# Kernel optimization log

Measured on AMD Instinct MI355X. Metric: run time of the kernel, lower is better.

## Reference

```python
import jax, jax.numpy as jnp
import numpy as np
from jax.scipy.special import betaln

B, T = 4096, 8192

def setup_inputs() -> dict:
    key = jax.random.key(0)
    k_obs, k_a1, k_b1, k_a2, k_b2 = jax.random.split(key, 5)
    obs_seq = (jax.random.uniform(k_obs, (B, T)) < 0.5).astype(jnp.float32)
    # priors strictly positive, away from 0 to keep betaln finite
    alpha1 = jax.random.uniform(k_a1, (B,)) * 2.0 + 0.5
    beta1 = jax.random.uniform(k_b1, (B,)) * 2.0 + 0.5
    alpha2 = jax.random.uniform(k_a2, (B,)) * 2.0 + 0.5
    beta2 = jax.random.uniform(k_b2, (B,)) * 2.0 + 0.5
    mixweight = jnp.float32(0.4)
    return {"obs_seq": obs_seq, "alpha1": alpha1, "beta1": beta1,
            "alpha2": alpha2, "beta2": beta2, "mixweight": mixweight}

def reference(obs_seq, alpha1, beta1, alpha2, beta2, mixweight):
    # cumulative successes/failures, shifted right by one (posterior BEFORE obs t)
    cs = jnp.cumsum(obs_seq, axis=1)          # [B,T]
    cf = jnp.cumsum(1.0 - obs_seq, axis=1)    # [B,T]
    s_prev = jnp.pad(cs[:, :-1], ((0, 0), (1, 0)))  # cat([0, cs[:-1]])
    f_prev = jnp.pad(cf[:, :-1], ((0, 0), (1, 0)))
    a1 = alpha1[:, None] + s_prev
    b1 = beta1[:, None] + f_prev
    a2 = alpha2[:, None] + s_prev
    b2 = beta2[:, None] + f_prev
    clog1 = betaln(a1, b1) - betaln(alpha1, beta1)[:, None]
    clog2 = betaln(a2, b2) - betaln(alpha2, beta2)[:, None]
    bigconst = -clog1
    c1 = mixweight * jnp.exp(clog1 + bigconst)
    c2 = (1.0 - mixweight) * jnp.exp(clog2 + bigconst)
    post_mixweight = c1 / (c1 + c2)
    # stack the post_dict entries into one [5,B,T] array
    return jnp.stack([a1, b1, a2, b2, post_mixweight])
```

## Files before the change

### kernel.cpp

```cpp
#include <hip/hip_runtime.h>


#define BLOCK 256
#define VEC 4
#define NW (BLOCK / 64)

typedef float v4f __attribute__((ext_vector_type(4)));

__global__ __launch_bounds__(BLOCK) void bbm_kernel(
    const float* __restrict__ obs,
    const float* __restrict__ alpha1, const float* __restrict__ beta1,
    const float* __restrict__ alpha2, const float* __restrict__ beta2,
    const float* __restrict__ mixw,
    float* __restrict__ out,
    int T, size_t bt)
{
    const int bid   = blockIdx.x;
    const int row   = bid / 5;
    const int plane = bid - row * 5;
    const int tid   = threadIdx.x;
    const int lane  = tid & 63;
    const int wid   = tid >> 6;

    __shared__ int   sPart[2][NW];
    __shared__ float dPart[2][NW];

    const float* __restrict__ orow = obs + (size_t)row * T;
    float* __restrict__ prow = out + (size_t)plane * bt + (size_t)row * T;

    const unsigned long long lt_mask = ((unsigned long long)1 << lane) - 1ull;

    const int EPB   = BLOCK * VEC;
    const int iters = T / EPB;

    v4f cur = *(const v4f*)(orow + tid * VEC);

    if (plane < 4) {
        const float A1 = alpha1[row], B1 = beta1[row];
        const float A2 = alpha2[row], B2 = beta2[row];
        const float c0 = (plane == 0) ? A1 : (plane == 1) ? B1
                       : (plane == 2) ? A2 : B2;
        const bool use_s = (plane & 1) == 0;

        int carry_s = 0;
        for (int it = 0; it < iters; ++it) {
            const int t0 = it * EPB + tid * VEC;
            const int pb = it & 1;

            v4f nxt;
            if (it + 1 < iters) nxt = *(const v4f*)(orow + (it + 1) * EPB + tid * VEC);

            int bit[VEC], sloc[VEC];
            int ts = 0;
            #pragma unroll
            for (int j = 0; j < VEC; ++j) { bit[j] = cur[j] > 0.5f; sloc[j] = ts; ts += bit[j]; }

            unsigned long long m0 = __ballot(bit[0]);
            unsigned long long m1 = __ballot(bit[1]);
            unsigned long long m2 = __ballot(bit[2]);
            unsigned long long m3 = __ballot(bit[3]);
            const int wave_excl = __builtin_popcountll(m0 & lt_mask)
                                + __builtin_popcountll(m1 & lt_mask)
                                + __builtin_popcountll(m2 & lt_mask)
                                + __builtin_popcountll(m3 & lt_mask);
            const int wave_tot  = __builtin_popcountll(m0) + __builtin_popcountll(m1)
                                + __builtin_popcountll(m2) + __builtin_popcountll(m3);
            if (lane == 0) sPart[pb][wid] = wave_tot;
            __syncthreads();
            int prior = 0, total = 0;
            #pragma unroll
            for (int wI = 0; wI < NW; ++wI) {
                int p = sPart[pb][wI];
                total += p;
                if (wI < wid) prior += p;
            }
            const int tbase_s = carry_s + prior + wave_excl;

            v4f o;
            #pragma unroll
            for (int j = 0; j < VEC; ++j) {
                const float ft = (float)(t0 + j);
                const float fs = (float)(tbase_s + sloc[j]);
                o[j] = use_s ? (c0 + fs) : (c0 + (ft - fs));
            }
            *(v4f*)(prow + t0) = o;

            carry_s += total;
            cur = nxt;
        }
    } else {
        const float A1 = alpha1[row], B1 = beta1[row];
        const float A2 = alpha2[row], B2 = beta2[row];
        const float w  = mixw[0];
        const float AB1 = A1 + B1, AB2 = A2 + B2;
        const float w2 = 1.0f - w;

        int   carry_s = 0;
        float carry_d = 0.0f;

        for (int it = 0; it < iters; ++it) {
            const int t0 = it * EPB + tid * VEC;
            const int pb = it & 1;

            v4f nxt;
            if (it + 1 < iters) nxt = *(const v4f*)(orow + (it + 1) * EPB + tid * VEC);

            int bit[VEC], sloc[VEC];
            int ts = 0;
            #pragma unroll
            for (int j = 0; j < VEC; ++j) { bit[j] = cur[j] > 0.5f; sloc[j] = ts; ts += bit[j]; }

            unsigned long long m0 = __ballot(bit[0]);
            unsigned long long m1 = __ballot(bit[1]);
            unsigned long long m2 = __ballot(bit[2]);
            unsigned long long m3 = __ballot(bit[3]);
            const int wave_excl = __builtin_popcountll(m0 & lt_mask)
                                + __builtin_popcountll(m1 & lt_mask)
                                + __builtin_popcountll(m2 & lt_mask)
                                + __builtin_popcountll(m3 & lt_mask);
            const int wave_tot  = __builtin_popcountll(m0) + __builtin_popcountll(m1)
                                + __builtin_popcountll(m2) + __builtin_popcountll(m3);
            if (lane == 0) sPart[pb][wid] = wave_tot;
            __syncthreads();
            int prior = 0, total = 0;
            #pragma unroll
            for (int wI = 0; wI < NW; ++wI) {
                int p = sPart[pb][wI];
                total += p;
                if (wI < wid) prior += p;
            }
            const int tbase_s = carry_s + prior + wave_excl;

            float dloc[VEC];
            float td = 0.0f;
            #pragma unroll
            for (int j = 0; j < VEC; ++j) {
                const float ft = (float)(t0 + j);
                const float fs = (float)(tbase_s + sloc[j]);
                const float fp = ft - fs;
                const float sel1 = bit[j] ? (A1 + fs) : (B1 + fp);
                const float sel2 = bit[j] ? (A2 + fs) : (B2 + fp);
                const float delta = __logf(sel2 * (AB1 + ft)) - __logf(sel1 * (AB2 + ft));
                dloc[j] = td;
                td += delta;
            }

            float incl_d = td;
            #pragma unroll
            for (int off = 1; off < 64; off <<= 1) {
                float n = __shfl_up(incl_d, off, 64);
                if (lane >= off) incl_d += n;
            }
            if (lane == 63) dPart[pb][wid] = incl_d;
            __syncthreads();
            float priord = 0.0f, totald = 0.0f;
            #pragma unroll
            for (int wI = 0; wI < NW; ++wI) {
                float p = dPart[pb][wI];
                totald += p;
                if (wI < wid) priord += p;
            }
            const float tbase_d = carry_d + priord + (incl_d - td);

            v4f o;
            #pragma unroll
            for (int j = 0; j < VEC; ++j) {
                const float d = tbase_d + dloc[j];
                o[j] = __fdividef(w, w + w2 * __expf(d));
            }
            *(v4f*)(prow + t0) = o;

            carry_s += total;
            carry_d += totald;
            cur = nxt;
        }
    }
}

extern "C" void kernel_launch(void* const* d_in, const int* in_sizes, int n_in,
                              void* d_out, int out_size, void* d_ws, size_t ws_size,
                              hipStream_t stream) {
    const float* obs    = (const float*)d_in[0];
    const float* alpha1 = (const float*)d_in[1];
    const float* beta1  = (const float*)d_in[2];
    const float* alpha2 = (const float*)d_in[3];
    const float* beta2  = (const float*)d_in[4];
    const float* mixw   = (const float*)d_in[5];

    const int Bn = in_sizes[1];
    const int Tn = in_sizes[0] / Bn;
    const size_t bt = (size_t)Bn * (size_t)Tn;

    bbm_kernel<<<Bn * 5, BLOCK, 0, stream>>>(obs, alpha1, beta1, alpha2, beta2,
                                             mixw, (float*)d_out, Tn, bt);
}
```

Baseline: 795.4 us.

## Fuse five output planes into one block per row with staggered plane stores

Instead of launching five blocks per row that each redo the scan and write one plane, one block per row now computes all five outputs. This removes four redundant reads of obs and repeated scans. A templated fully unrolled variant for T equal to 8 segments delays each plane's store by a different number of segments, so the concurrent stores are spread across planes and addresses. The cost is fewer blocks in the grid (B instead of 5B), more live registers for the delayed buffers, and a heavier sequential chain per block.

```diff
diff --git a/kernel.cpp b/kernel.cpp
--- a/kernel.cpp
+++ b/kernel.cpp
@@ -7,7 +7,8 @@
 
 typedef float v4f __attribute__((ext_vector_type(4)));
 
-__global__ __launch_bounds__(BLOCK) void bbm_kernel(
+template <int SEGS>
+__global__ __launch_bounds__(BLOCK) void bbm_lag(
     const float* __restrict__ obs,
     const float* __restrict__ alpha1, const float* __restrict__ beta1,
     const float* __restrict__ alpha2, const float* __restrict__ beta2,
@@ -15,40 +16,44 @@
     float* __restrict__ out,
     int T, size_t bt)
 {
-    const int bid   = blockIdx.x;
-    const int row   = bid / 5;
-    const int plane = bid - row * 5;
-    const int tid   = threadIdx.x;
-    const int lane  = tid & 63;
-    const int wid   = tid >> 6;
+    const int row  = blockIdx.x;
+    const int tid  = threadIdx.x;
+    const int lane = tid & 63;
+    const int wid  = tid >> 6;
 
     __shared__ int   sPart[2][NW];
     __shared__ float dPart[2][NW];
 
+    const float A1 = alpha1[row], B1 = beta1[row];
+    const float A2 = alpha2[row], B2 = beta2[row];
+    const float w  = mixw[0];
+    const float AB1 = A1 + B1, AB2 = A2 + B2;
+    const float w2 = 1.0f - w;
+
     const float* __restrict__ orow = obs + (size_t)row * T;
-    float* __restrict__ prow = out + (size_t)plane * bt + (size_t)row * T;
+    float* __restrict__ obase = out + (size_t)row * T;
 
     const unsigned long long lt_mask = ((unsigned long long)1 << lane) - 1ull;
 
-    const int EPB   = BLOCK * VEC;
-    const int iters = T / EPB;
+    int   carry_s = 0;
+    float carry_d = 0.0f;
+
+    const int EPB = BLOCK * VEC;
+
+    v4f fb1[1], fa2[2], fb2[3], fpm[4];
 
     v4f cur = *(const v4f*)(orow + tid * VEC);
 
-    if (plane < 4) {
-        const float A1 = alpha1[row], B1 = beta1[row];
-        const float A2 = alpha2[row], B2 = beta2[row];
-        const float c0 = (plane == 0) ? A1 : (plane == 1) ? B1
-                       : (plane == 2) ? A2 : B2;
-        const bool use_s = (plane & 1) == 0;
-
-        int carry_s = 0;
-        for (int it = 0; it < iters; ++it) {
-            const int t0 = it * EPB + tid * VEC;
-            const int pb = it & 1;
+    #pragma unroll
+    for (int s = 0; s < SEGS + 4; ++s) {
+        v4f va1, vb1n, va2n, vb2n, vpmn;
+
+        if (s < SEGS) {
+            const int t0 = s * EPB + tid * VEC;
+            const int pb = s & 1;
 
             v4f nxt;
-            if (it + 1 < iters) nxt = *(const v4f*)(orow + (it + 1) * EPB + tid * VEC);
+            if (s + 1 < SEGS) nxt = *(const v4f*)(orow + (s + 1) * EPB + tid * VEC);
 
             int bit[VEC], sloc[VEC];
             int ts = 0;
@@ -76,61 +81,6 @@
             }
             const int tbase_s = carry_s + prior + wave_excl;
 
-            v4f o;
-            #pragma unroll
-            for (int j = 0; j < VEC; ++j) {
-                const float ft = (float)(t0 + j);
-                const float fs = (float)(tbase_s + sloc[j]);
-                o[j] = use_s ? (c0 + fs) : (c0 + (ft - fs));
-            }
-            *(v4f*)(prow + t0) = o;
-
-            carry_s += total;
-            cur = nxt;
-        }
-    } else {
-        const float A1 = alpha1[row], B1 = beta1[row];
-        const float A2 = alpha2[row], B2 = beta2[row];
-        const float w  = mixw[0];
-        const float AB1 = A1 + B1, AB2 = A2 + B2;
-        const float w2 = 1.0f - w;
-
-        int   carry_s = 0;
-        float carry_d = 0.0f;
-
-        for (int it = 0; it < iters; ++it) {
-            const int t0 = it * EPB + tid * VEC;
-            const int pb = it & 1;
-
-            v4f nxt;
-            if (it + 1 < iters) nxt = *(const v4f*)(orow + (it + 1) * EPB + tid * VEC);
-
-            int bit[VEC], sloc[VEC];
-            int ts = 0;
-            #pragma unroll
-            for (int j = 0; j < VEC; ++j) { bit[j] = cur[j] > 0.5f; sloc[j] = ts; ts += bit[j]; }
-
-            unsigned long long m0 = __ballot(bit[0]);
-            unsigned long long m1 = __ballot(bit[1]);
-            unsigned long long m2 = __ballot(bit[2]);
-            unsigned long long m3 = __ballot(bit[3]);
-            const int wave_excl = __builtin_popcountll(m0 & lt_mask)
-                                + __builtin_popcountll(m1 & lt_mask)
-                                + __builtin_popcountll(m2 & lt_mask)
-                                + __builtin_popcountll(m3 & lt_mask);
-            const int wave_tot  = __builtin_popcountll(m0) + __builtin_popcountll(m1)
-                                + __builtin_popcountll(m2) + __builtin_popcountll(m3);
-            if (lane == 0) sPart[pb][wid] = wave_tot;
-            __syncthreads();
-            int prior = 0, total = 0;
-            #pragma unroll
-            for (int wI = 0; wI < NW; ++wI) {
-                int p = sPart[pb][wI];
-                total += p;
-                if (wI < wid) prior += p;
-            }
-            const int tbase_s = carry_s + prior + wave_excl;
-
             float dloc[VEC];
             float td = 0.0f;
             #pragma unroll
@@ -162,18 +112,165 @@
             }
             const float tbase_d = carry_d + priord + (incl_d - td);
 
-            v4f o;
             #pragma unroll
             for (int j = 0; j < VEC; ++j) {
-                const float d = tbase_d + dloc[j];
-                o[j] = __fdividef(w, w + w2 * __expf(d));
-            }
-            *(v4f*)(prow + t0) = o;
+                const float ft = (float)(t0 + j);
+                const float fs = (float)(tbase_s + sloc[j]);
+                const float fp = ft - fs;
+                const float d  = tbase_d + dloc[j];
+                va1[j]  = A1 + fs;
+                vb1n[j] = B1 + fp;
+                va2n[j] = A2 + fs;
+                vb2n[j] = B2 + fp;
+                vpmn[j] = __fdividef(w, w + w2 * __expf(d));
+            }
+            *(v4f*)(obase + t0) = va1;
 
             carry_s += total;
             carry_d += totald;
             cur = nxt;
         }
+
+        if (s - 1 >= 0 && s - 1 < SEGS)
+            *(v4f*)(obase + bt     + (size_t)(s - 1) * EPB + tid * VEC) = fb1[0];
+        if (s - 2 >= 0 && s - 2 < SEGS)
+            *(v4f*)(obase + 2 * bt + (size_t)(s - 2) * EPB + tid * VEC) = fa2[s & 1];
+        if (s - 3 >= 0 && s - 3 < SEGS)
+            *(v4f*)(obase + 3 * bt + (size_t)(s - 3) * EPB + tid * VEC) = fb2[s % 3];
+        if (s - 4 >= 0 && s - 4 < SEGS)
+            *(v4f*)(obase + 4 * bt + (size_t)(s - 4) * EPB + tid * VEC) = fpm[s & 3];
+
+        if (s < SEGS) {
+            fb1[0]     = vb1n;
+            fa2[s & 1] = va2n;
+            fb2[s % 3] = vb2n;
+            fpm[s & 3] = vpmn;
+        }
+    }
+}
+
+__global__ __launch_bounds__(BLOCK) void bbm_kernel(
+    const float* __restrict__ obs,
+    const float* __restrict__ alpha1, const float* __restrict__ beta1,
+    const float* __restrict__ alpha2, const float* __restrict__ beta2,
+    const float* __restrict__ mixw,
+    float* __restrict__ out,
+    int T, size_t bt)
+{
+    const int row  = blockIdx.x;
+    const int tid  = threadIdx.x;
+    const int lane = tid & 63;
+    const int wid  = tid >> 6;
+
+    __shared__ int   sPart[2][NW];
+    __shared__ float dPart[2][NW];
+
+    const float A1 = alpha1[row], B1 = beta1[row];
+    const float A2 = alpha2[row], B2 = beta2[row];
+    const float w  = mixw[0];
+    const float AB1 = A1 + B1, AB2 = A2 + B2;
+    const float w2 = 1.0f - w;
+
+    const float* __restrict__ orow = obs + (size_t)row * T;
+    float* __restrict__ obase = out + (size_t)row * T;
+
+    const unsigned long long lt_mask = ((unsigned long long)1 << lane) - 1ull;
+
+    int   carry_s = 0;
+    float carry_d = 0.0f;
+
+    const int EPB  = BLOCK * VEC;
+    const int segs = T / EPB;
+
+    v4f cur = *(const v4f*)(orow + tid * VEC);
+
+    for (int s = 0; s < segs; ++s) {
+        const int t0 = s * EPB + tid * VEC;
+        const int pb = s & 1;
+
+        v4f nxt;
+        if (s + 1 < segs) nxt = *(const v4f*)(orow + (s + 1) * EPB + tid * VEC);
+
+        int bit[VEC], sloc[VEC];
+        int ts = 0;
+        #pragma unroll
+        for (int j = 0; j < VEC; ++j) { bit[j] = cur[j] > 0.5f; sloc[j] = ts; ts += bit[j]; }
+
+        unsigned long long m0 = __ballot(bit[0]);
+        unsigned long long m1 = __ballot(bit[1]);
+        unsigned long long m2 = __ballot(bit[2]);
+        unsigned long long m3 = __ballot(bit[3]);
+        const int wave_excl = __builtin_popcountll(m0 & lt_mask)
+                            + __builtin_popcountll(m1 & lt_mask)
+                            + __builtin_popcountll(m2 & lt_mask)
+                            + __builtin_popcountll(m3 & lt_mask);
+        const int wave_tot  = __builtin_popcountll(m0) + __builtin_popcountll(m1)
+                            + __builtin_popcountll(m2) + __builtin_popcountll(m3);
+        if (lane == 0) sPart[pb][wid] = wave_tot;
+        __syncthreads();
+        int prior = 0, total = 0;
+        #pragma unroll
+        for (int wI = 0; wI < NW; ++wI) {
+            int p = sPart[pb][wI];
+            total += p;
+            if (wI < wid) prior += p;
+        }
+        const int tbase_s = carry_s + prior + wave_excl;
+
+        float dloc[VEC];
+        float td = 0.0f;
+        #pragma unroll
+        for (int j = 0; j < VEC; ++j) {
+            const float ft = (float)(t0 + j);
+            const float fs = (float)(tbase_s + sloc[j]);
+            const float fp = ft - fs;
+            const float sel1 = bit[j] ? (A1 + fs) : (B1 + fp);
+            const float sel2 = bit[j] ? (A2 + fs) : (B2 + fp);
+            const float delta = __logf(sel2 * (AB1 + ft)) - __logf(sel1 * (AB2 + ft));
+            dloc[j] = td;
+            td += delta;
+        }
+
+        float incl_d = td;
+        #pragma unroll
+        for (int off = 1; off < 64; off <<= 1) {
+            float n = __shfl_up(incl_d, off, 64);
+            if (lane >= off) incl_d += n;
+        }
+        if (lane == 63) dPart[pb][wid] = incl_d;
+        __syncthreads();
+        float priord = 0.0f, totald = 0.0f;
+        #pragma unroll
+        for (int wI = 0; wI < NW; ++wI) {
+            float p = dPart[pb][wI];
+            totald += p;
+            if (wI < wid) priord += p;
+        }
+        const float tbase_d = carry_d + priord + (incl_d - td);
+
+        v4f va1, vb1, va2, vb2, vpm;
+        #pragma unroll
+        for (int j = 0; j < VEC; ++j) {
+            const float ft = (float)(t0 + j);
+            const float fs = (float)(tbase_s + sloc[j]);
+            const float fp = ft - fs;
+            const float d  = tbase_d + dloc[j];
+            va1[j] = A1 + fs;
+            vb1[j] = B1 + fp;
+            va2[j] = A2 + fs;
+            vb2[j] = B2 + fp;
+            vpm[j] = __fdividef(w, w + w2 * __expf(d));
+        }
+        float* p = obase + t0;
+        *(v4f*)(p)          = va1;
+        *(v4f*)(p + bt)     = vb1;
+        *(v4f*)(p + 2 * bt) = va2;
+        *(v4f*)(p + 3 * bt) = vb2;
+        *(v4f*)(p + 4 * bt) = vpm;
+
+        carry_s += total;
+        carry_d += totald;
+        cur = nxt;
     }
 }
 
@@ -191,6 +288,12 @@
     const int Tn = in_sizes[0] / Bn;
     const size_t bt = (size_t)Bn * (size_t)Tn;
 
-    bbm_kernel<<<Bn * 5, BLOCK, 0, stream>>>(obs, alpha1, beta1, alpha2, beta2,
+    const int EPB = BLOCK * VEC;
+    if (Tn == 8 * EPB) {
+        bbm_lag<8><<<Bn, BLOCK, 0, stream>>>(obs, alpha1, beta1, alpha2, beta2,
                                              mixw, (float*)d_out, Tn, bt);
+    } else {
+        bbm_kernel<<<Bn, BLOCK, 0, stream>>>(obs, alpha1, beta1, alpha2, beta2,
+                                             mixw, (float*)d_out, Tn, bt);
+    }
 }
```

Result: faster. 742.1 us (-6.7%).
